# Kernel optimization log

Measured on AMD Instinct MI355X. Metric: run time of the kernel, lower is better.

## Reference

```python
import jax, jax.numpy as jnp
import numpy as np

B, T, C, H, L, V = 64, 256, 256, 8, 6, 96
EPS = 1e-5


def _layernorm(x, w, b):
    m = x.mean(-1, keepdims=True)
    v = x.var(-1, keepdims=True)
    return (x - m) / jnp.sqrt(v + EPS) * w + b


def setup_inputs() -> dict:
    key = jax.random.key(0)
    ks = jax.random.split(key, 16)
    s = 0.05
    n = lambda k, sh: jax.random.normal(k, sh, jnp.float32) * s
    return {
        'idx': jax.random.randint(ks[0], (B, T), 0, V),
        'target': jax.random.randint(ks[1], (B, T), 0, V),
        'tok_emb': n(ks[2], (V, C)),
        'pos_emb': n(ks[3], (T, C)),
        'Wq': n(ks[4], (L, C, C)),
        'Wk': n(ks[5], (L, C, C)),
        'Wv': n(ks[6], (L, C, C)),
        'Wo': n(ks[7], (L, C, C)),
        'bo': jnp.zeros((L, C), jnp.float32),
        'W1': n(ks[8], (L, C, C)),
        'b1': jnp.zeros((L, C), jnp.float32),
        'W2': n(ks[9], (L, C, C)),
        'b2': jnp.zeros((L, C), jnp.float32),
        'ln1_w': jnp.ones((L, C), jnp.float32),
        'ln1_b': jnp.zeros((L, C), jnp.float32),
        'ln2_w': jnp.ones((L, C), jnp.float32),
        'ln2_b': jnp.zeros((L, C), jnp.float32),
        'lnf_w': jnp.ones((C,), jnp.float32),
        'lnf_b': jnp.zeros((C,), jnp.float32),
        'Wlm': n(ks[10], (C, V)),
        'blm': jnp.zeros((V,), jnp.float32),
    }


def _forward(idx, target, tok_emb, pos_emb, Wq, Wk, Wv, Wo, bo, W1, b1, W2, b2,
             ln1_w, ln1_b, ln2_w, ln2_b, lnf_w, lnf_b, Wlm, blm):
    Bc, Tc = idx.shape
    hs = C // H
    scale = C ** (-0.5)  # NOTE: original scales by n_embed**-0.5, not head_size**-0.5
    x = tok_emb[idx] + pos_emb[:Tc]              # [B,T,C]
    causal = jnp.tril(jnp.ones((Tc, Tc), bool))  # [T,T]
    for l in range(L):
        q = (x @ Wq[l]).reshape(Bc, Tc, H, hs)
        k = (x @ Wk[l]).reshape(Bc, Tc, H, hs)
        v = (x @ Wv[l]).reshape(Bc, Tc, H, hs)
        w = jnp.einsum('bqhd,bkhd->bhqk', q, k) * scale
        w = jnp.where(causal, w, -jnp.inf)
        w = jax.nn.softmax(w, axis=-1)
        att = jnp.einsum('bhqk,bkhd->bqhd', w, v).reshape(Bc, Tc, C)
        x = _layernorm(x + att @ Wo[l] + bo[l], ln1_w[l], ln1_b[l])  # post-residual LN
        h = jax.nn.relu(x @ W1[l] + b1[l]) @ W2[l] + b2[l]
        x = _layernorm(x + h, ln2_w[l], ln2_b[l])
    x = _layernorm(x, lnf_w, lnf_b)
    logits = (x @ Wlm + blm).reshape(Bc * Tc, V)
    logp = jax.nn.log_softmax(logits, axis=-1)
    nll = -jnp.take_along_axis(logp, target.reshape(-1, 1), axis=1)
    loss = nll.mean()
    return logits, loss


def reference(idx, target, tok_emb, pos_emb, Wq, Wk, Wv, Wo, bo, W1, b1, W2, b2,
              ln1_w, ln1_b, ln2_w, ln2_b, lnf_w, lnf_b, Wlm, blm):
    return _forward(idx, target, tok_emb, pos_emb, Wq, Wk, Wv, Wo, bo, W1, b1, W2, b2,
                    ln1_w, ln1_b, ln2_w, ln2_b, lnf_w, lnf_b, Wlm, blm)
```

## Files before the change

kernel.cpp:

```cpp
#include <hip/hip_runtime.h>

typedef unsigned short u16;

#define NT   16384
#define LAYERS 6

using bf16x8 = __attribute__((ext_vector_type(8))) __bf16;
using f32x4  = __attribute__((ext_vector_type(4))) float;

#define MFMA __builtin_amdgcn_mfma_f32_16x16x32_bf16

__device__ __forceinline__ u16 f2bf(float x){
  unsigned u = __float_as_uint(x);
  u += 0x7fffu + ((u >> 16) & 1u);
  return (u16)(u >> 16);
}
__device__ __forceinline__ float bf2f(u16 u){
  return __uint_as_float(((unsigned)u) << 16);
}

__device__ __forceinline__ void gll16(const u16* g, u16* l){
  __builtin_amdgcn_global_load_lds(
      (const __attribute__((address_space(1))) unsigned int*)g,
      (__attribute__((address_space(3))) unsigned int*)l, 16, 0, 0);
}

__global__ __launch_bounds__(256) void wconv_k(
    const float* __restrict__ Wq, const float* __restrict__ Wk,
    const float* __restrict__ Wv, const float* __restrict__ Wo,
    const float* __restrict__ W1, const float* __restrict__ W2,
    const float* __restrict__ Wlm, u16* __restrict__ WT)
{
  __shared__ float tile[64][65];
  const int z = blockIdx.z;
  const float* src; u16* dst; int N = 256, Npad = 256;
  if (z < 18){
    const int l = z / 3, which = z % 3;
    const float* a[3] = {Wq, Wk, Wv};
    src = a[which] + (size_t)l * 65536;
    dst = WT + (size_t)l * 196608 + (size_t)which * 65536;
  } else if (z < 36){
    const int i = z - 18, j = i / 6, l = i % 6;
    const float* a[3] = {Wo, W1, W2};
    src = a[j] + (size_t)l * 65536;
    dst = WT + 1179648 + (size_t)(j * 6 + l) * 65536;
  } else {
    src = Wlm; dst = WT + 2359296; N = 96; Npad = 128;
  }
  const int n0 = blockIdx.y * 64, k0 = blockIdx.x * 64;
  if (n0 >= Npad) return;
  const int c = threadIdx.x & 63, r0 = threadIdx.x >> 6;
  #pragma unroll
  for (int i = 0; i < 16; ++i){
    const int r = r0 + i * 4;
    tile[r][c] = (n0 + c < N) ? src[(size_t)(k0 + r) * N + n0 + c] : 0.f;
  }
  __syncthreads();
  #pragma unroll
  for (int i = 0; i < 16; ++i){
    const int cp = r0 + i * 4;
    dst[(size_t)(n0 + cp) * 256 + k0 + c] = f2bf(tile[c][cp]);
  }
}

__global__ __launch_bounds__(256) void embed_k(
    const int* __restrict__ idx, const float* __restrict__ tok,
    const float* __restrict__ pos, u16* __restrict__ X)
{
  const int w = threadIdx.x >> 6, l = threadIdx.x & 63;
  const int r = blockIdx.x * 4 + w;
  const int id = idx[r];
  float4 tv = *reinterpret_cast<const float4*>(tok + (size_t)id * 256 + l * 4);
  float4 pv = *reinterpret_cast<const float4*>(pos + (size_t)(r & 255) * 256 + l * 4);
  union { u16 u[4]; uint2 q; } p;
  p.u[0] = f2bf(tv.x + pv.x); p.u[1] = f2bf(tv.y + pv.y);
  p.u[2] = f2bf(tv.z + pv.z); p.u[3] = f2bf(tv.w + pv.w);
  *reinterpret_cast<uint2*>(X + (size_t)r * 256 + l * 4) = p.q;
}

template<int TM, int TN, int THREADS, int WR, int WC,
         bool BIAS, bool RELU, bool RES, bool LN, bool F32OUT>
__global__ __launch_bounds__(THREADS) void gemm3_k(
    const u16* __restrict__ A, const u16* __restrict__ WT,
    const float* __restrict__ bias, const u16* __restrict__ res,
    void* __restrict__ outp, const float* __restrict__ lnw,
    const float* __restrict__ lnb, int N, int ldo)
{
  constexpr int MR = TM / (WR * 16), NR = TN / (WC * 16);
  extern __shared__ char smem[];
  u16* As = (u16*)smem;
  u16* Bs = As + 2 * TM * 64;
  float* redS = (float*)(Bs + 2 * TN * 64);
  float* redQ = redS + TM * (WC + 1);

  const int t = threadIdx.x, l = t & 63, w = t >> 6;
  const int wr = w / WC, wc = w % WC;
  const int m0 = blockIdx.x * TM, n0 = blockIdx.y * TN;
  const int lr = l & 15, lk = (l >> 4) * 8, rj = (l >> 4) * 4;
  const int rb = wr * (TM / WR), cb = wc * (TN / WC);
  f32x4 acc[MR][NR] = {};

  auto stage = [&](int buf, int kt){
    const int k0 = kt * 64;
    u16* as = As + buf * (TM * 64);
    u16* bs = Bs + buf * (TN * 64);
    #pragma unroll
    for (int ci = t; ci < TM * 8; ci += THREADS){
      const int eo = ci * 8;
      gll16(A + (size_t)(m0 + (eo >> 6)) * 256 + k0 + (eo & 63), as + eo);
    }
    #pragma unroll
    for (int ci = t; ci < TN * 8; ci += THREADS){
      const int eo = ci * 8;
      gll16(WT + (size_t)(n0 + (eo >> 6)) * 256 + k0 + (eo & 63), bs + eo);
    }
  };
  auto compute = [&](int buf){
    const u16* as = As + buf * (TM * 64);
    const u16* bs = Bs + buf * (TN * 64);
    #pragma unroll
    for (int kk = 0; kk < 64; kk += 32){
      bf16x8 af[MR], bf[NR];
      #pragma unroll
      for (int m = 0; m < MR; ++m)
        af[m] = *reinterpret_cast<const bf16x8*>(&as[(rb + m*16 + lr) * 64 + kk + lk]);
      #pragma unroll
      for (int n = 0; n < NR; ++n)
        bf[n] = *reinterpret_cast<const bf16x8*>(&bs[(cb + n*16 + lr) * 64 + kk + lk]);
      #pragma unroll
      for (int m = 0; m < MR; ++m)
        #pragma unroll
        for (int n = 0; n < NR; ++n)
          acc[m][n] = MFMA(af[m], bf[n], acc[m][n], 0, 0, 0);
    }
  };

  stage(0, 0);
  __syncthreads();
  #pragma unroll
  for (int kt = 0; kt < 4; ++kt){
    if (kt < 3) stage((kt + 1) & 1, kt + 1);
    compute(kt & 1);
    if (kt < 3) __syncthreads();
  }

  if constexpr (LN){
    #pragma unroll
    for (int m = 0; m < MR; ++m){
      #pragma unroll
      for (int j = 0; j < 4; ++j){
        const int lrow = rb + m*16 + rj + j;
        const int grow = m0 + lrow;
        float s = 0.f, q = 0.f;
        #pragma unroll
        for (int n = 0; n < NR; ++n){
          const int gcol = cb + n*16 + lr;
          float v = acc[m][n][j] + bias[gcol] + bf2f(res[(size_t)grow * 256 + gcol]);
          acc[m][n][j] = v;
          s += v; q += v * v;
        }
        #pragma unroll
        for (int o = 1; o < 16; o <<= 1){ s += __shfl_xor(s, o); q += __shfl_xor(q, o); }
        if (lr == 0){ redS[lrow*(WC+1) + wc] = s; redQ[lrow*(WC+1) + wc] = q; }
      }
    }
    __syncthreads();
    #pragma unroll
    for (int m = 0; m < MR; ++m){
      #pragma unroll
      for (int j = 0; j < 4; ++j){
        const int lrow = rb + m*16 + rj + j;
        const int grow = m0 + lrow;
        float s = 0.f, q = 0.f;
        #pragma unroll
        for (int c = 0; c < WC; ++c){ s += redS[lrow*(WC+1) + c]; q += redQ[lrow*(WC+1) + c]; }
        const float mean = s * (1.f/256.f);
        const float rstd = rsqrtf(q * (1.f/256.f) - mean*mean + 1e-5f);
        #pragma unroll
        for (int n = 0; n < NR; ++n){
          const int gcol = cb + n*16 + lr;
          ((u16*)outp)[(size_t)grow * 256 + gcol] =
              f2bf((acc[m][n][j] - mean) * rstd * lnw[gcol] + lnb[gcol]);
        }
      }
    }
  } else {
    #pragma unroll
    for (int m = 0; m < MR; ++m){
      #pragma unroll
      for (int n = 0; n < NR; ++n){
        const int gcol = n0 + cb + n*16 + lr;
        if (gcol < N){
          #pragma unroll
          for (int j = 0; j < 4; ++j){
            const int grow = m0 + rb + m*16 + rj + j;
            const size_t o = (size_t)grow * ldo + gcol;
            float v = acc[m][n][j];
            if (BIAS) v += bias[gcol];
            if (RES)  v += bf2f(res[o]);
            if (RELU) v = fmaxf(v, 0.f);
            if (F32OUT) ((float*)outp)[o] = v;
            else        ((u16*)outp)[o] = f2bf(v);
          }
        }
      }
    }
  }
}

__global__ __launch_bounds__(256) void attn2_k(
    const u16* __restrict__ QKV, u16* __restrict__ O)
{
  extern __shared__ char smem[];
  u16* Ks = (u16*)smem;
  u16* Qs = Ks + 256 * 40;
  u16* VT = Qs + 64 * 40;
  u16* Ps = VT + 32 * 264;

  const int bh = blockIdx.x, b = bh >> 3, h = bh & 7;
  const size_t rbase = (size_t)b * 256 * 768;
  const int qc = h * 32, kc = 256 + h * 32, vc = 512 + h * 32;
  const int t = threadIdx.x, l = t & 63, w = t >> 6;
  const int lr = l & 15, lk = (l >> 4) * 8, rj = (l >> 4) * 4;
  const int r4 = t >> 2, c8 = (t & 3) * 8;

  #pragma unroll
  for (int it = 0; it < 4; ++it){
    const int row = it * 64 + r4;
    *reinterpret_cast<uint4*>(Ks + row * 40 + c8) =
        *reinterpret_cast<const uint4*>(QKV + rbase + (size_t)row * 768 + kc + c8);
    union { uint4 q; u16 u[8]; } p;
    p.q = *reinterpret_cast<const uint4*>(QKV + rbase + (size_t)row * 768 + vc + c8);
    #pragma unroll
    for (int j2 = 0; j2 < 8; ++j2) VT[(c8 + j2) * 264 + row] = p.u[j2];
  }
  __syncthreads();

  bf16x8 kf[16];
  #pragma unroll
  for (int n = 0; n < 16; ++n)
    kf[n] = *reinterpret_cast<const bf16x8*>(Ks + (n*16 + lr) * 40 + lk);

  #pragma unroll 1
  for (int c = 0; c < 4; ++c){
    *reinterpret_cast<uint4*>(Qs + r4 * 40 + c8) =
        *reinterpret_cast<const uint4*>(QKV + rbase + (size_t)(c*64 + r4) * 768 + qc + c8);
    __syncthreads();

    bf16x8 qa = *reinterpret_cast<const bf16x8*>(Qs + (w*16 + lr) * 40 + lk);
    const int nmax = 4 * (c + 1);
    f32x4 s[16];
    #pragma unroll
    for (int n = 0; n < 16; ++n){
      if (n < nmax){ f32x4 z = {}; s[n] = MFMA(qa, kf[n], z, 0, 0, 0); }
    }
    float inv[4];
    #pragma unroll
    for (int j = 0; j < 4; ++j){
      const int tq = c*64 + w*16 + rj + j;
      float m = -1e30f;
      #pragma unroll
      for (int n = 0; n < 16; ++n){
        if (n < nmax){
          float v = s[n][j] * 0.0625f;
          v = ((n*16 + lr) <= tq) ? v : -1e30f;
          s[n][j] = v;
          m = fmaxf(m, v);
        }
      }
      #pragma unroll
      for (int o = 1; o < 16; o <<= 1) m = fmaxf(m, __shfl_xor(m, o));
      float sum = 0.f;
      #pragma unroll
      for (int n = 0; n < 16; ++n){
        if (n < nmax){
          const float p = __expf(s[n][j] - m);
          sum += p;
          Ps[(w*16 + rj + j) * 264 + n*16 + lr] = f2bf(p);
        }
      }
      #pragma unroll
      for (int o = 1; o < 16; o <<= 1) sum += __shfl_xor(sum, o);
      inv[j] = 1.f / sum;
    }
    __syncthreads();

    f32x4 o0 = {}, o1 = {};
    #pragma unroll
    for (int k2 = 0; k2 < 8; ++k2){
      if (k2 < 2 * (c + 1)){
        bf16x8 pa  = *reinterpret_cast<const bf16x8*>(Ps + (w*16 + lr) * 264 + k2*32 + lk);
        bf16x8 vb0 = *reinterpret_cast<const bf16x8*>(VT + lr * 264 + k2*32 + lk);
        bf16x8 vb1 = *reinterpret_cast<const bf16x8*>(VT + (16 + lr) * 264 + k2*32 + lk);
        o0 = MFMA(pa, vb0, o0, 0, 0, 0);
        o1 = MFMA(pa, vb1, o1, 0, 0, 0);
      }
    }
    #pragma unroll
    for (int j = 0; j < 4; ++j){
      const int row = c*64 + w*16 + rj + j;
      u16* op = O + (size_t)(b*256 + row) * 256 + h*32;
      op[lr]      = f2bf(o0[j] * inv[j]);
      op[16 + lr] = f2bf(o1[j] * inv[j]);
    }
    __syncthreads();
  }
}

__global__ __launch_bounds__(256) void lnf_k(
    const u16* __restrict__ in, const float* __restrict__ w,
    const float* __restrict__ b, u16* __restrict__ out)
{
  const int wv = threadIdx.x >> 6, l = threadIdx.x & 63;
  const int r = blockIdx.x * 4 + wv;
  union { uint2 q; u16 u[4]; } iv;
  iv.q = *reinterpret_cast<const uint2*>(in + (size_t)r * 256 + l * 4);
  float v0 = bf2f(iv.u[0]), v1 = bf2f(iv.u[1]), v2 = bf2f(iv.u[2]), v3 = bf2f(iv.u[3]);
  float s = v0 + v1 + v2 + v3;
  float q = v0*v0 + v1*v1 + v2*v2 + v3*v3;
  #pragma unroll
  for (int o = 32; o; o >>= 1){ s += __shfl_xor(s, o); q += __shfl_xor(q, o); }
  const float mean = s * (1.f/256.f);
  const float rstd = rsqrtf(q * (1.f/256.f) - mean*mean + 1e-5f);
  float4 w4 = *reinterpret_cast<const float4*>(w + l * 4);
  float4 b4 = *reinterpret_cast<const float4*>(b + l * 4);
  union { u16 u[4]; uint2 q2; } p;
  p.u[0] = f2bf((v0 - mean) * rstd * w4.x + b4.x);
  p.u[1] = f2bf((v1 - mean) * rstd * w4.y + b4.y);
  p.u[2] = f2bf((v2 - mean) * rstd * w4.z + b4.z);
  p.u[3] = f2bf((v3 - mean) * rstd * w4.w + b4.w);
  *reinterpret_cast<uint2*>(out + (size_t)r * 256 + l * 4) = p.q2;
}

__global__ __launch_bounds__(256) void nll_k(
    const float* __restrict__ logits, const int* __restrict__ target,
    float* __restrict__ nll)
{
  const int w = threadIdx.x >> 6, l = threadIdx.x & 63;
  const int r = blockIdx.x * 4 + w;
  const float* row = logits + (size_t)r * 96;
  float v0 = row[l];
  float v1 = (l < 32) ? row[64 + l] : -1e30f;
  float m = fmaxf(v0, v1);
  #pragma unroll
  for (int o = 32; o; o >>= 1) m = fmaxf(m, __shfl_xor(m, o));
  float s = __expf(v0 - m) + ((l < 32) ? __expf(v1 - m) : 0.f);
  #pragma unroll
  for (int o = 32; o; o >>= 1) s += __shfl_xor(s, o);
  if (l == 0) nll[r] = logf(s) + m - row[target[r]];
}

__global__ __launch_bounds__(256) void loss_k(
    const float* __restrict__ nll, float* __restrict__ out)
{
  __shared__ float rs[4];
  float s = 0.f;
  for (int i = threadIdx.x; i < NT; i += 256) s += nll[i];
  #pragma unroll
  for (int o = 32; o; o >>= 1) s += __shfl_xor(s, o);
  if ((threadIdx.x & 63) == 0) rs[threadIdx.x >> 6] = s;
  __syncthreads();
  if (threadIdx.x == 0) out[0] = (rs[0] + rs[1] + rs[2] + rs[3]) * (1.f / 16384.f);
}

extern "C" void kernel_launch(void* const* d_in, const int* in_sizes, int n_in,
                              void* d_out, int out_size, void* d_ws, size_t ws_size,
                              hipStream_t stream)
{
  const int*   idx    = (const int*)  d_in[0];
  const int*   target = (const int*)  d_in[1];
  const float* tok    = (const float*)d_in[2];
  const float* pos    = (const float*)d_in[3];
  const float* bo     = (const float*)d_in[8];
  const float* b1     = (const float*)d_in[10];
  const float* b2     = (const float*)d_in[12];
  const float* ln1w   = (const float*)d_in[13];
  const float* ln1b   = (const float*)d_in[14];
  const float* ln2w   = (const float*)d_in[15];
  const float* ln2b   = (const float*)d_in[16];
  const float* lnfw   = (const float*)d_in[17];
  const float* lnfb   = (const float*)d_in[18];
  const float* blm    = (const float*)d_in[20];
  float* out = (float*)d_out;

  char* ws = (char*)d_ws;
  u16*   X   = (u16*)(ws);
  u16*   QKV = (u16*)(ws + ( 8u << 20));
  u16*   O   = (u16*)(ws + (32u << 20));
  u16*   hB  = (u16*)(ws + (40u << 20));
  u16*   Xf  = (u16*)(ws + (48u << 20));
  u16*   WT  = (u16*)(ws + (56u << 20));
  float* nl  = (float*)(ws + (62u << 20));

  const size_t SM_QKV = (size_t)2*(128+128)*64*2 + 2*128*5*4;
  const size_t SM_LN  = (size_t)2*(64+256)*64*2 + 2*64*9*4;
  const size_t SM_W1  = (size_t)2*(64+128)*64*2 + 2*64*5*4;
  const size_t SM_AT  = (size_t)(256*40 + 64*40 + 32*264 + 64*264) * 2;

  wconv_k<<<dim3(4, 4, 37), 256, 0, stream>>>(
      (const float*)d_in[4], (const float*)d_in[5], (const float*)d_in[6],
      (const float*)d_in[7], (const float*)d_in[9], (const float*)d_in[11],
      (const float*)d_in[19], WT);
  embed_k<<<NT / 4, 256, 0, stream>>>(idx, tok, pos, X);

  for (int l = 0; l < LAYERS; ++l){
    const u16* wqkv = WT + (size_t)l * 196608;
    const u16* wo   = WT + 1179648 + (size_t)(0*6 + l) * 65536;
    const u16* w1   = WT + 1179648 + (size_t)(1*6 + l) * 65536;
    const u16* w2   = WT + 1179648 + (size_t)(2*6 + l) * 65536;

    gemm3_k<128,128,512,2,4, false,false,false,false,false>
        <<<dim3(128, 6), 512, SM_QKV, stream>>>(
        X, wqkv, nullptr, nullptr, QKV, nullptr, nullptr, 768, 768);
    attn2_k<<<512, 256, SM_AT, stream>>>(QKV, O);
    gemm3_k<64,256,1024,2,8, true,false,true,true,false>
        <<<dim3(256, 1), 1024, SM_LN, stream>>>(
        O, wo, bo + l*256, X, X, ln1w + l*256, ln1b + l*256, 256, 256);
    gemm3_k<64,128,512,2,4, true,true,false,false,false>
        <<<dim3(256, 2), 512, SM_W1, stream>>>(
        X, w1, b1 + l*256, nullptr, hB, nullptr, nullptr, 256, 256);
    gemm3_k<64,256,1024,2,8, true,false,true,true,false>
        <<<dim3(256, 1), 1024, SM_LN, stream>>>(
        hB, w2, b2 + l*256, X, X, ln2w + l*256, ln2b + l*256, 256, 256);
  }

  lnf_k<<<NT / 4, 256, 0, stream>>>(X, lnfw, lnfb, Xf);
  gemm3_k<64,128,512,2,4, true,false,false,false,true>
      <<<dim3(256, 1), 512, SM_W1, stream>>>(
      Xf, WT + 2359296, blm, nullptr, out, nullptr, nullptr, 96, 96);
  nll_k<<<NT / 4, 256, 0, stream>>>(out, target, nl);
  loss_k<<<1, 256, 0, stream>>>(nl, out + (size_t)NT * 96);
}
```

Measured before the change: 620.4 us.

## Fuse LN-epilogue GEMMs with the following GEMM (FFN1, next-layer QKV, LM head)

Adds a two-stage kernel, gemmF_k. It first computes a 64-row GEMM with bias, residual and LayerNorm, keeps the normalized rows in LDS, and then runs a second GEMM against them. This fuses Wo+LN1 with W1+ReLU, W2+LN2 with the next layer's QKV projection, and the last layer's W2+LN2 with the final LN and the LM head. The standalone QKV launch per layer, the lnf kernel and the separate FFN1/LM-head launches go away, saving launches and global round trips of X. The trade-off is a large LDS footprint per 1024-thread block, and the 3-chunk QKV pass serializes the 768-wide output within one block, which may reduce parallelism.

```diff
diff --git a/kernel.cpp b/kernel.cpp
--- a/kernel.cpp
+++ b/kernel.cpp
@@ -78,20 +78,15 @@
   *reinterpret_cast<uint2*>(X + (size_t)r * 256 + l * 4) = p.q;
 }
 
-template<int TM, int TN, int THREADS, int WR, int WC,
-         bool BIAS, bool RELU, bool RES, bool LN, bool F32OUT>
+template<int TM, int TN, int THREADS, int WR, int WC>
 __global__ __launch_bounds__(THREADS) void gemm3_k(
     const u16* __restrict__ A, const u16* __restrict__ WT,
-    const float* __restrict__ bias, const u16* __restrict__ res,
-    void* __restrict__ outp, const float* __restrict__ lnw,
-    const float* __restrict__ lnb, int N, int ldo)
+    u16* __restrict__ outp, int ldo)
 {
   constexpr int MR = TM / (WR * 16), NR = TN / (WC * 16);
   extern __shared__ char smem[];
   u16* As = (u16*)smem;
   u16* Bs = As + 2 * TM * 64;
-  float* redS = (float*)(Bs + 2 * TN * 64);
-  float* redQ = redS + TM * (WC + 1);
 
   const int t = threadIdx.x, l = t & 63, w = t >> 6;
   const int wr = w / WC, wc = w % WC;
@@ -120,18 +115,18 @@
     const u16* bs = Bs + buf * (TN * 64);
     #pragma unroll
     for (int kk = 0; kk < 64; kk += 32){
-      bf16x8 af[MR], bf[NR];
+      bf16x8 af[MR], bfv[NR];
       #pragma unroll
       for (int m = 0; m < MR; ++m)
         af[m] = *reinterpret_cast<const bf16x8*>(&as[(rb + m*16 + lr) * 64 + kk + lk]);
       #pragma unroll
       for (int n = 0; n < NR; ++n)
-        bf[n] = *reinterpret_cast<const bf16x8*>(&bs[(cb + n*16 + lr) * 64 + kk + lk]);
+        bfv[n] = *reinterpret_cast<const bf16x8*>(&bs[(cb + n*16 + lr) * 64 + kk + lk]);
       #pragma unroll
       for (int m = 0; m < MR; ++m)
         #pragma unroll
         for (int n = 0; n < NR; ++n)
-          acc[m][n] = MFMA(af[m], bf[n], acc[m][n], 0, 0, 0);
+          acc[m][n] = MFMA(af[m], bfv[n], acc[m][n], 0, 0, 0);
     }
   };
 
@@ -143,64 +138,199 @@
     compute(kt & 1);
     if (kt < 3) __syncthreads();
   }
-
-  if constexpr (LN){
-    #pragma unroll
-    for (int m = 0; m < MR; ++m){
+  #pragma unroll
+  for (int m = 0; m < MR; ++m)
+    #pragma unroll
+    for (int n = 0; n < NR; ++n){
+      const int gcol = n0 + cb + n*16 + lr;
       #pragma unroll
       for (int j = 0; j < 4; ++j){
-        const int lrow = rb + m*16 + rj + j;
-        const int grow = m0 + lrow;
-        float s = 0.f, q = 0.f;
+        const int grow = m0 + rb + m*16 + rj + j;
+        outp[(size_t)grow * ldo + gcol] = f2bf(acc[m][n][j]);
+      }
+    }
+}
+
+template<int TN2, int NCH, bool RELU2, bool BIAS2, bool LNF, bool F32O2>
+__global__ __launch_bounds__(1024) void gemmF_k(
+    const u16* __restrict__ A, const u16* __restrict__ Bw1,
+    const float* __restrict__ bias1, u16* __restrict__ X,
+    const float* __restrict__ lnw, const float* __restrict__ lnb,
+    const u16* __restrict__ Bw2, const float* __restrict__ bias2,
+    void* __restrict__ out2, int ldo2,
+    const float* __restrict__ lnfw, const float* __restrict__ lnfb)
+{
+  constexpr int NR2 = TN2 / 128;
+  extern __shared__ char smem[];
+  u16* As = (u16*)smem;
+  u16* Bs = As + 8192;
+  u16* Xn = Bs + 32768;
+  float* redS = (float*)(Xn + 16896);
+  float* redQ = redS + 64 * 9;
+
+  const int t = threadIdx.x, l = t & 63, w = t >> 6;
+  const int wr = w >> 3, wc = w & 7;
+  const int m0 = blockIdx.x * 64;
+  const int lr = l & 15, lk = (l >> 4) * 8, rj = (l >> 4) * 4;
+  const int rb = wr * 32, cb = wc * 32;
+  const int cb2 = wc * (TN2 / 8);
+
+  auto stage1 = [&](int buf, int kt){
+    const int k0 = kt * 64;
+    u16* as = As + buf * 4096;
+    u16* bs = Bs + buf * 16384;
+    if (t < 512){
+      const int eo = t * 8;
+      gll16(A + (size_t)(m0 + (eo >> 6)) * 256 + k0 + (eo & 63), as + eo);
+    }
+    #pragma unroll
+    for (int i = 0; i < 2; ++i){
+      const int eo = (i * 1024 + t) * 8;
+      gll16(Bw1 + (size_t)(eo >> 6) * 256 + k0 + (eo & 63), bs + eo);
+    }
+  };
+  auto stage2 = [&](int buf, int nc, int kt){
+    const int k0 = kt * 64;
+    u16* bs = Bs + buf * 16384;
+    #pragma unroll
+    for (int i = 0; i < TN2 / 128; ++i){
+      const int eo = (i * 1024 + t) * 8;
+      gll16(Bw2 + (size_t)(nc * TN2 + (eo >> 6)) * 256 + k0 + (eo & 63), bs + eo);
+    }
+  };
+
+  f32x4 acc[2][2] = {};
+  stage1(0, 0);
+  __syncthreads();
+  #pragma unroll
+  for (int kt = 0; kt < 4; ++kt){
+    if (kt < 3) stage1((kt + 1) & 1, kt + 1);
+    const u16* as = As + (kt & 1) * 4096;
+    const u16* bs = Bs + (kt & 1) * 16384;
+    #pragma unroll
+    for (int kk = 0; kk < 64; kk += 32){
+      bf16x8 af[2], bfv[2];
+      #pragma unroll
+      for (int m = 0; m < 2; ++m)
+        af[m] = *reinterpret_cast<const bf16x8*>(&as[(rb + m*16 + lr) * 64 + kk + lk]);
+      #pragma unroll
+      for (int n = 0; n < 2; ++n)
+        bfv[n] = *reinterpret_cast<const bf16x8*>(&bs[(cb + n*16 + lr) * 64 + kk + lk]);
+      #pragma unroll
+      for (int m = 0; m < 2; ++m)
         #pragma unroll
-        for (int n = 0; n < NR; ++n){
-          const int gcol = cb + n*16 + lr;
-          float v = acc[m][n][j] + bias[gcol] + bf2f(res[(size_t)grow * 256 + gcol]);
-          acc[m][n][j] = v;
-          s += v; q += v * v;
-        }
+        for (int n = 0; n < 2; ++n)
+          acc[m][n] = MFMA(af[m], bfv[n], acc[m][n], 0, 0, 0);
+    }
+    if (kt < 3) __syncthreads();
+  }
+
+  stage2(0, 0, 0);
+
+  #pragma unroll
+  for (int m = 0; m < 2; ++m){
+    #pragma unroll
+    for (int j = 0; j < 4; ++j){
+      const int lrow = rb + m*16 + rj + j;
+      float s = 0.f, q = 0.f;
+      #pragma unroll
+      for (int n = 0; n < 2; ++n){
+        const int col = cb + n*16 + lr;
+        float v = acc[m][n][j] + bias1[col] + bf2f(X[(size_t)(m0 + lrow) * 256 + col]);
+        acc[m][n][j] = v;
+        s += v; q += v * v;
+      }
+      #pragma unroll
+      for (int o = 1; o < 16; o <<= 1){ s += __shfl_xor(s, o); q += __shfl_xor(q, o); }
+      if (lr == 0){ redS[lrow*9 + wc] = s; redQ[lrow*9 + wc] = q; }
+    }
+  }
+  __syncthreads();
+  #pragma unroll
+  for (int m = 0; m < 2; ++m){
+    #pragma unroll
+    for (int j = 0; j < 4; ++j){
+      const int lrow = rb + m*16 + rj + j;
+      float s = 0.f, q = 0.f;
+      #pragma unroll
+      for (int c = 0; c < 8; ++c){ s += redS[lrow*9 + c]; q += redQ[lrow*9 + c]; }
+      const float mean = s * (1.f/256.f);
+      const float rstd = rsqrtf(q * (1.f/256.f) - mean*mean + 1e-5f);
+      #pragma unroll
+      for (int n = 0; n < 2; ++n){
+        const int col = cb + n*16 + lr;
+        const u16 y = f2bf((acc[m][n][j] - mean) * rstd * lnw[col] + lnb[col]);
+        Xn[lrow*264 + col] = y;
+        X[(size_t)(m0 + lrow) * 256 + col] = y;
+      }
+    }
+  }
+
+  if constexpr (LNF){
+    __syncthreads();
+    #pragma unroll
+    for (int rr = 0; rr < 4; ++rr){
+      const int row = w * 4 + rr;
+      union { uint2 q2; u16 u[4]; } iv;
+      iv.q2 = *reinterpret_cast<const uint2*>(Xn + row*264 + l*4);
+      float v0 = bf2f(iv.u[0]), v1 = bf2f(iv.u[1]), v2 = bf2f(iv.u[2]), v3 = bf2f(iv.u[3]);
+      float s = v0 + v1 + v2 + v3;
+      float q = v0*v0 + v1*v1 + v2*v2 + v3*v3;
+      #pragma unroll
+      for (int o = 1; o < 64; o <<= 1){ s += __shfl_xor(s, o); q += __shfl_xor(q, o); }
+      const float mean = s * (1.f/256.f);
+      const float rstd = rsqrtf(q * (1.f/256.f) - mean*mean + 1e-5f);
+      union { u16 u[4]; uint2 q2; } p;
+      p.u[0] = f2bf((v0 - mean) * rstd * lnfw[l*4+0] + lnfb[l*4+0]);
+      p.u[1] = f2bf((v1 - mean) * rstd * lnfw[l*4+1] + lnfb[l*4+1]);
+      p.u[2] = f2bf((v2 - mean) * rstd * lnfw[l*4+2] + lnfb[l*4+2]);
+      p.u[3] = f2bf((v3 - mean) * rstd * lnfw[l*4+3] + lnfb[l*4+3]);
+      *reinterpret_cast<uint2*>(Xn + row*264 + l*4) = p.q2;
+    }
+  }
+  __syncthreads();
+
+  #pragma unroll 1
+  for (int nc = 0; nc < NCH; ++nc){
+    f32x4 a2[2][NR2] = {};
+    #pragma unroll
+    for (int kt = 0; kt < 4; ++kt){
+      const int s = nc*4 + kt, nx = s + 1;
+      if (nx < NCH*4) stage2(nx & 1, nx >> 2, nx & 3);
+      const u16* bs = Bs + (s & 1) * 16384;
+      #pragma unroll
+      for (int kk2 = 0; kk2 < 64; kk2 += 32){
+        const int kk = kt*64 + kk2;
+        bf16x8 af[2], bfv[NR2];
         #pragma unroll
-        for (int o = 1; o < 16; o <<= 1){ s += __shfl_xor(s, o); q += __shfl_xor(q, o); }
-        if (lr == 0){ redS[lrow*(WC+1) + wc] = s; redQ[lrow*(WC+1) + wc] = q; }
-      }
-    }
-    __syncthreads();
-    #pragma unroll
-    for (int m = 0; m < MR; ++m){
-      #pragma unroll
-      for (int j = 0; j < 4; ++j){
-        const int lrow = rb + m*16 + rj + j;
-        const int grow = m0 + lrow;
-        float s = 0.f, q = 0.f;
+        for (int m = 0; m < 2; ++m)
+          af[m] = *reinterpret_cast<const bf16x8*>(Xn + (rb + m*16 + lr)*264 + kk + lk);
         #pragma unroll
-        for (int c = 0; c < WC; ++c){ s += redS[lrow*(WC+1) + c]; q += redQ[lrow*(WC+1) + c]; }
-        const float mean = s * (1.f/256.f);
-        const float rstd = rsqrtf(q * (1.f/256.f) - mean*mean + 1e-5f);
+        for (int n = 0; n < NR2; ++n)
+          bfv[n] = *reinterpret_cast<const bf16x8*>(&bs[(cb2 + n*16 + lr)*64 + kk2 + lk]);
         #pragma unroll
-        for (int n = 0; n < NR; ++n){
-          const int gcol = cb + n*16 + lr;
-          ((u16*)outp)[(size_t)grow * 256 + gcol] =
-              f2bf((acc[m][n][j] - mean) * rstd * lnw[gcol] + lnb[gcol]);
-        }
-      }
-    }
-  } else {
-    #pragma unroll
-    for (int m = 0; m < MR; ++m){
-      #pragma unroll
-      for (int n = 0; n < NR; ++n){
-        const int gcol = n0 + cb + n*16 + lr;
-        if (gcol < N){
+        for (int m = 0; m < 2; ++m)
           #pragma unroll
-          for (int j = 0; j < 4; ++j){
-            const int grow = m0 + rb + m*16 + rj + j;
-            const size_t o = (size_t)grow * ldo + gcol;
-            float v = acc[m][n][j];
-            if (BIAS) v += bias[gcol];
-            if (RES)  v += bf2f(res[o]);
-            if (RELU) v = fmaxf(v, 0.f);
-            if (F32OUT) ((float*)outp)[o] = v;
-            else        ((u16*)outp)[o] = f2bf(v);
+          for (int n = 0; n < NR2; ++n)
+            a2[m][n] = MFMA(af[m], bfv[n], a2[m][n], 0, 0, 0);
+      }
+      if (nx < NCH*4) __syncthreads();
+    }
+    #pragma unroll
+    for (int m = 0; m < 2; ++m){
+      #pragma unroll
+      for (int n = 0; n < NR2; ++n){
+        const int col = nc*TN2 + cb2 + n*16 + lr;
+        #pragma unroll
+        for (int j = 0; j < 4; ++j){
+          const int grow = m0 + rb + m*16 + rj + j;
+          float v = a2[m][n][j];
+          if (BIAS2) v += bias2[col];
+          if (RELU2) v = fmaxf(v, 0.f);
+          if (F32O2){
+            if (col < 96) ((float*)out2)[(size_t)grow * ldo2 + col] = v;
+          } else {
+            ((u16*)out2)[(size_t)grow * ldo2 + col] = f2bf(v);
           }
         }
       }
@@ -305,31 +435,6 @@
     }
     __syncthreads();
   }
-}
-
-__global__ __launch_bounds__(256) void lnf_k(
-    const u16* __restrict__ in, const float* __restrict__ w,
-    const float* __restrict__ b, u16* __restrict__ out)
-{
-  const int wv = threadIdx.x >> 6, l = threadIdx.x & 63;
-  const int r = blockIdx.x * 4 + wv;
-  union { uint2 q; u16 u[4]; } iv;
-  iv.q = *reinterpret_cast<const uint2*>(in + (size_t)r * 256 + l * 4);
-  float v0 = bf2f(iv.u[0]), v1 = bf2f(iv.u[1]), v2 = bf2f(iv.u[2]), v3 = bf2f(iv.u[3]);
-  float s = v0 + v1 + v2 + v3;
-  float q = v0*v0 + v1*v1 + v2*v2 + v3*v3;
-  #pragma unroll
-  for (int o = 32; o; o >>= 1){ s += __shfl_xor(s, o); q += __shfl_xor(q, o); }
-  const float mean = s * (1.f/256.f);
-  const float rstd = rsqrtf(q * (1.f/256.f) - mean*mean + 1e-5f);
-  float4 w4 = *reinterpret_cast<const float4*>(w + l * 4);
-  float4 b4 = *reinterpret_cast<const float4*>(b + l * 4);
-  union { u16 u[4]; uint2 q2; } p;
-  p.u[0] = f2bf((v0 - mean) * rstd * w4.x + b4.x);
-  p.u[1] = f2bf((v1 - mean) * rstd * w4.y + b4.y);
-  p.u[2] = f2bf((v2 - mean) * rstd * w4.z + b4.z);
-  p.u[3] = f2bf((v3 - mean) * rstd * w4.w + b4.w);
-  *reinterpret_cast<uint2*>(out + (size_t)r * 256 + l * 4) = p.q2;
 }
 
 __global__ __launch_bounds__(256) void nll_k(
@@ -388,14 +493,12 @@
   u16*   QKV = (u16*)(ws + ( 8u << 20));
   u16*   O   = (u16*)(ws + (32u << 20));
   u16*   hB  = (u16*)(ws + (40u << 20));
-  u16*   Xf  = (u16*)(ws + (48u << 20));
-  u16*   WT  = (u16*)(ws + (56u << 20));
-  float* nl  = (float*)(ws + (62u << 20));
-
-  const size_t SM_QKV = (size_t)2*(128+128)*64*2 + 2*128*5*4;
-  const size_t SM_LN  = (size_t)2*(64+256)*64*2 + 2*64*9*4;
-  const size_t SM_W1  = (size_t)2*(64+128)*64*2 + 2*64*5*4;
+  u16*   WT  = (u16*)(ws + (48u << 20));
+  float* nl  = (float*)(ws + (56u << 20));
+
+  const size_t SM_QKV = (size_t)2*(128+128)*64*2;
   const size_t SM_AT  = (size_t)(256*40 + 64*40 + 32*264 + 64*264) * 2;
+  const size_t SM_F   = (size_t)(8192 + 32768 + 16896)*2 + 64*9*4*2;
 
   wconv_k<<<dim3(4, 4, 37), 256, 0, stream>>>(
       (const float*)d_in[4], (const float*)d_in[5], (const float*)d_in[6],
@@ -403,31 +506,31 @@
       (const float*)d_in[19], WT);
   embed_k<<<NT / 4, 256, 0, stream>>>(idx, tok, pos, X);
 
+  gemm3_k<128,128,512,2,4><<<dim3(128, 6), 512, SM_QKV, stream>>>(
+      X, WT, QKV, 768);
+
   for (int l = 0; l < LAYERS; ++l){
-    const u16* wqkv = WT + (size_t)l * 196608;
-    const u16* wo   = WT + 1179648 + (size_t)(0*6 + l) * 65536;
-    const u16* w1   = WT + 1179648 + (size_t)(1*6 + l) * 65536;
-    const u16* w2   = WT + 1179648 + (size_t)(2*6 + l) * 65536;
-
-    gemm3_k<128,128,512,2,4, false,false,false,false,false>
-        <<<dim3(128, 6), 512, SM_QKV, stream>>>(
-        X, wqkv, nullptr, nullptr, QKV, nullptr, nullptr, 768, 768);
+    const u16* wo = WT + 1179648 + (size_t)(0*6 + l) * 65536;
+    const u16* w1 = WT + 1179648 + (size_t)(1*6 + l) * 65536;
+    const u16* w2 = WT + 1179648 + (size_t)(2*6 + l) * 65536;
+
     attn2_k<<<512, 256, SM_AT, stream>>>(QKV, O);
-    gemm3_k<64,256,1024,2,8, true,false,true,true,false>
-        <<<dim3(256, 1), 1024, SM_LN, stream>>>(
-        O, wo, bo + l*256, X, X, ln1w + l*256, ln1b + l*256, 256, 256);
-    gemm3_k<64,128,512,2,4, true,true,false,false,false>
-        <<<dim3(256, 2), 512, SM_W1, stream>>>(
-        X, w1, b1 + l*256, nullptr, hB, nullptr, nullptr, 256, 256);
-    gemm3_k<64,256,1024,2,8, true,false,true,true,false>
-        <<<dim3(256, 1), 1024, SM_LN, stream>>>(
-        hB, w2, b2 + l*256, X, X, ln2w + l*256, ln2b + l*256, 256, 256);
-  }
-
-  lnf_k<<<NT / 4, 256, 0, stream>>>(X, lnfw, lnfb, Xf);
-  gemm3_k<64,128,512,2,4, true,false,false,false,true>
-      <<<dim3(256, 1), 512, SM_W1, stream>>>(
-      Xf, WT + 2359296, blm, nullptr, out, nullptr, nullptr, 96, 96);
+
+    gemmF_k<256,1,true,true,false,false><<<256, 1024, SM_F, stream>>>(
+        O, wo, bo + l*256, X, ln1w + l*256, ln1b + l*256,
+        w1, b1 + l*256, hB, 256, nullptr, nullptr);
+
+    if (l < LAYERS - 1){
+      gemmF_k<256,3,false,false,false,false><<<256, 1024, SM_F, stream>>>(
+          hB, w2, b2 + l*256, X, ln2w + l*256, ln2b + l*256,
+          WT + (size_t)(l+1) * 196608, nullptr, QKV, 768, nullptr, nullptr);
+    } else {
+      gemmF_k<128,1,false,true,true,true><<<256, 1024, SM_F, stream>>>(
+          hB, w2, b2 + l*256, X, ln2w + l*256, ln2b + l*256,
+          WT + 2359296, blm, out, 96, lnfw, lnfb);
+    }
+  }
+
   nll_k<<<NT / 4, 256, 0, stream>>>(out, target, nl);
   loss_k<<<1, 256, 0, stream>>>(nl, out + (size_t)NT * 96);
 }
```

New measurement: 584.4 us. -5.8%, faster.
